# Optimization experiments

Measured on AMD Instinct MI355X. Metric: run time of the kernel, lower is better.

Reference implementation:

```python
import jax, jax.numpy as jnp
import numpy as np

SIGMA_AGG = 0.5
NUM_SEG = 33  # labels in [0, 32]; 0 = background


def setup_inputs() -> dict:
    key = jax.random.key(0)
    k1, k2, k3, k4, k5 = jax.random.split(key, 5)
    B, C, H, W = 16, 4, 736, 736
    return {
        "pred_similarities": jax.random.normal(k1, (B, C, H, W), dtype=jnp.float32),
        "regions_mask": jax.random.uniform(k2, (B, 1, H, W), dtype=jnp.float32),
        "kernels_mask": jax.random.uniform(k3, (B, 1, H, W), dtype=jnp.float32),
        "text_mask_ndi_labels": jax.random.randint(k4, (B, 1, H, W), 0, NUM_SEG, dtype=jnp.int32),
        "kernel_mask_ndi_labels": jax.random.randint(k5, (B, 1, H, W), 0, NUM_SEG, dtype=jnp.int32),
    }


def _per_batch(pred, rmask, kmask, rlab, klab):
    # pred: [C, N]; rmask/kmask: [N]; rlab/klab: [N] int
    # Per-kernel-label sum of kernels_mask, scattered back; 0 where label==0.
    ksum = jax.ops.segment_sum(kmask, klab, num_segments=NUM_SEG)            # [S]
    kcard = jnp.where(klab > 0, ksum[klab], 0.0)                              # [N]
    # Per-kernel-label sum of pred_similarities per channel.
    psum = jax.ops.segment_sum(pred.T, klab, num_segments=NUM_SEG)            # [S, C]
    Gk = jnp.where(klab[None, :] > 0, psum[klab].T, 0.0)                      # [C, N]
    # Region cardinality: faithful to source, it sums kernels_mask (not regions_mask)
    # over region labels.
    rsum = jax.ops.segment_sum(kmask, rlab, num_segments=NUM_SEG)             # [S]
    rcard = jnp.where(rlab > 0, rsum[rlab], 0.0)                              # [N]
    return kcard, Gk, rcard


def reference(pred_similarities, regions_mask, kernels_mask,
              text_mask_ndi_labels, kernel_mask_ndi_labels):
    B, C, H, W = pred_similarities.shape
    N = H * W
    pred = pred_similarities.reshape(B, C, N)
    rmask = regions_mask.reshape(B, N)
    kmask = kernels_mask.reshape(B, N)
    rlab = text_mask_ndi_labels.reshape(B, N)
    klab = kernel_mask_ndi_labels.reshape(B, N)

    kcard, Gk, rcard = jax.vmap(_per_batch)(pred, rmask, kmask, rlab, klab)
    # kcard/rcard: [B, N], Gk: [B, C, N]

    Gk = Gk / (kcard[:, None, :] + 1.0)
    Fp = pred * rmask[:, None, :]
    norm = jnp.sqrt(jnp.sum((Fp - Gk) ** 2, axis=1))                          # [B, N]
    d = jnp.maximum(norm - SIGMA_AGG, 0.0)
    D_p_K = jnp.log(d ** 2 + 1.0) / (rcard + 1.0)
    # Faithful to source bug: num_kernel is the LAST batch's max kernel label.
    num_kernel = klab[-1].max().astype(D_p_K.dtype)
    L_agg = (D_p_K / num_kernel).sum()
    return L_agg
```

## Files before the change

### kernel.cpp

```cpp
#include <hip/hip_runtime.h>
#include <hip/hip_cooperative_groups.h>

namespace cg = cooperative_groups;


constexpr int NSEG = 33;
constexpr int NCH  = 4;
constexpr int WS_PER_B = NSEG * (NCH + 2);
constexpr float SIGMA_AGG = 0.5f;
constexpr float QSCALE = 32768.0f;
constexpr float QINV   = 1.0f / 32768.0f;
constexpr float P8SCALE = 16.0f;
constexpr float P8INV   = 1.0f / 16.0f;

constexpr int NUMK_OFF = 16 * WS_PER_B;
constexpr int PART_OFF = 3200;

constexpr int BX    = 32;
constexpr int BTH   = 256;
constexpr int NITER = 17;

__device__ __forceinline__ int q8(float x) {
    int q = __float2int_rn(x * P8SCALE);
    return min(max(q, -127), 127) & 255;
}
__device__ __forceinline__ int pk8(float a, float b, float c, float d) {
    return q8(a) | (q8(b) << 8) | (q8(c) << 16) | (q8(d) << 24);
}
__device__ __forceinline__ float sx8(int w, int k) {
    return (float)((w << (24 - 8 * k)) >> 24);
}
__device__ __forceinline__ int pk16(int lo, int hi) {
    return (lo & 0xFFFF) | (hi << 16);
}

__global__ __launch_bounds__(BTH, 2) void fused_kernel(
    const float* __restrict__ pred, const float* __restrict__ rmask,
    const float* __restrict__ kmask, const int* __restrict__ rlab,
    const int* __restrict__ klab, int* __restrict__ ws,
    int* __restrict__ numk_out, float* __restrict__ partials,
    int N, int ncol, int lastB)
{
    const int b   = blockIdx.y;
    const int bx  = blockIdx.x;
    const int tid = threadIdx.x;

    __shared__ int   s_acc[WS_PER_B];
    __shared__ uint  s_lab[NITER][BTH][2];
    __shared__ float s_gk[NCH * NSEG];
    __shared__ float s_rinv[NSEG];
    __shared__ float s_part[4];
    for (int j = tid; j < WS_PER_B; j += BTH) s_acc[j] = 0;
    __syncthreads();

    const int Nv = N >> 2;
    const float4* __restrict__ predv = (const float4*)(pred + (size_t)b * NCH * N);
    const float4* __restrict__ kmv   = (const float4*)(kmask + (size_t)b * N);
    const int4*   __restrict__ rlv   = (const int4*)(rlab + (size_t)b * N);
    const int4*   __restrict__ klv   = (const int4*)(klab + (size_t)b * N);

    int rp8[NITER][4];

    int mk = 0;
    #pragma unroll
    for (int it = 0; it < NITER; ++it) {
        const int col = it * BX + bx;
        if (col < ncol) {
            const int i = col * BTH + tid;
            float4 km = kmv[i];
            int4   kl = klv[i];
            int4   rl = rlv[i];
            float4 p0 = predv[0 * Nv + i];
            float4 p1 = predv[1 * Nv + i];
            float4 p2 = predv[2 * Nv + i];
            float4 p3 = predv[3 * Nv + i];

            #define PIX(sfx) do {                                             \
                int kl_ = kl.sfx, rl_ = rl.sfx;                               \
                int kq = __float2int_rn(km.sfx * QSCALE);                     \
                atomicAdd(&s_acc[kl_], kq);                                   \
                atomicAdd(&s_acc[NSEG + rl_], kq);                            \
                atomicAdd(&s_acc[2 * NSEG + 0 * NSEG + kl_],                  \
                          __float2int_rn(p0.sfx * QSCALE));                   \
                atomicAdd(&s_acc[2 * NSEG + 1 * NSEG + kl_],                  \
                          __float2int_rn(p1.sfx * QSCALE));                   \
                atomicAdd(&s_acc[2 * NSEG + 2 * NSEG + kl_],                  \
                          __float2int_rn(p2.sfx * QSCALE));                   \
                atomicAdd(&s_acc[2 * NSEG + 3 * NSEG + kl_],                  \
                          __float2int_rn(p3.sfx * QSCALE));                   \
                mk = max(mk, kl_);                                            \
            } while (0)
            PIX(x); PIX(y); PIX(z); PIX(w);
            #undef PIX

            rp8[it][0] = pk8(p0.x, p1.x, p2.x, p3.x);
            rp8[it][1] = pk8(p0.y, p1.y, p2.y, p3.y);
            rp8[it][2] = pk8(p0.z, p1.z, p2.z, p3.z);
            rp8[it][3] = pk8(p0.w, p1.w, p2.w, p3.w);
            s_lab[it][tid][0] = (uint)pk16(kl.x | (rl.x << 6),
                                           kl.y | (rl.y << 6));
            s_lab[it][tid][1] = (uint)pk16(kl.z | (rl.z << 6),
                                           kl.w | (rl.w << 6));
        }
    }
    __syncthreads();

    int* wsb = ws + b * WS_PER_B;
    for (int j = tid; j < WS_PER_B; j += BTH)
        atomicAdd(&wsb[j], s_acc[j]);

    if (b == lastB) {
        for (int off = 32; off > 0; off >>= 1)
            mk = max(mk, __shfl_down(mk, off));
        if ((tid & 63) == 0) atomicMax(numk_out, mk);
    }

    cg::this_grid().sync();

    for (int j = tid; j < NSEG; j += BTH) {
        int rv = __hip_atomic_load(&wsb[NSEG + j], __ATOMIC_RELAXED,
                                   __HIP_MEMORY_SCOPE_AGENT);
        float rs = (float)rv * QINV;
        s_rinv[j] = (j > 0) ? 1.0f / (rs + 1.0f) : 1.0f;
    }
    for (int j = tid; j < NCH * NSEG; j += BTH) {
        int s  = j % NSEG;
        int kv = __hip_atomic_load(&wsb[s], __ATOMIC_RELAXED,
                                   __HIP_MEMORY_SCOPE_AGENT);
        int pv = __hip_atomic_load(&wsb[2 * NSEG + j], __ATOMIC_RELAXED,
                                   __HIP_MEMORY_SCOPE_AGENT);
        float ks = (float)kv * QINV;
        float ps = (float)pv * QINV;
        s_gk[j] = (s > 0) ? ps / (ks + 1.0f) : 0.0f;
    }
    __syncthreads();

    const float4* __restrict__ rmv = (const float4*)(rmask + (size_t)b * N);
    float acc = 0.0f;
    #pragma unroll
    for (int it = 0; it < NITER; ++it) {
        const int col = it * BX + bx;
        if (col < ncol) {
            const int i = col * BTH + tid;
            float4 rm = rmv[i];
            uint lw0 = s_lab[it][tid][0];
            uint lw1 = s_lab[it][tid][1];
            #define PIXR(w, lab16, rm_) do {                             \
                int kl_ = (lab16) & 63, rl_ = ((lab16) >> 6) & 63;       \
                float rmn = (rm_) * P8INV;                               \
                float d0 = fmaf(sx8(w, 0), rmn, -s_gk[0 * NSEG + kl_]);  \
                float d1 = fmaf(sx8(w, 1), rmn, -s_gk[1 * NSEG + kl_]);  \
                float d2 = fmaf(sx8(w, 2), rmn, -s_gk[2 * NSEG + kl_]);  \
                float d3 = fmaf(sx8(w, 3), rmn, -s_gk[3 * NSEG + kl_]);  \
                float ss = d0*d0 + d1*d1 + d2*d2 + d3*d3;                \
                float nrm = sqrtf(ss);                                   \
                float dd = fmaxf(nrm - SIGMA_AGG, 0.0f);                 \
                acc += __logf(fmaf(dd, dd, 1.0f)) * s_rinv[rl_];         \
            } while (0)
            PIXR(rp8[it][0], (int)(lw0 & 0xFFFF), rm.x);
            PIXR(rp8[it][1], (int)(lw0 >> 16),    rm.y);
            PIXR(rp8[it][2], (int)(lw1 & 0xFFFF), rm.z);
            PIXR(rp8[it][3], (int)(lw1 >> 16),    rm.w);
            #undef PIXR
        }
    }

    for (int off = 32; off > 0; off >>= 1)
        acc += __shfl_down(acc, off);
    if ((tid & 63) == 0) s_part[tid >> 6] = acc;
    __syncthreads();
    if (tid == 0)
        partials[b * BX + bx] = s_part[0] + s_part[1] + s_part[2] + s_part[3];
}

__global__ __launch_bounds__(256) void seg_sums_kernel(
    const float* __restrict__ pred, const float* __restrict__ kmask,
    const int* __restrict__ rlab, const int* __restrict__ klab,
    int* __restrict__ ws, int* __restrict__ numk_out, int N, int lastB)
{
    const int b = blockIdx.y;
    __shared__ int s_acc[WS_PER_B];
    __shared__ int s_maxk;
    for (int j = threadIdx.x; j < WS_PER_B; j += blockDim.x) s_acc[j] = 0;
    if (threadIdx.x == 0) s_maxk = 0;
    __syncthreads();

    const size_t bN = (size_t)b * N;
    const int Nv = N >> 2;
    const float4* __restrict__ predv = (const float4*)(pred + (size_t)b * NCH * N);
    const float4* __restrict__ kmv   = (const float4*)(kmask + bN);
    const int4*   __restrict__ rlv   = (const int4*)(rlab + bN);
    const int4*   __restrict__ klv   = (const int4*)(klab + bN);

    int mk = 0;
    for (int i = blockIdx.x * blockDim.x + threadIdx.x; i < Nv;
         i += gridDim.x * blockDim.x) {
        float4 km = kmv[i];
        int4   kl = klv[i];
        int4   rl = rlv[i];
        float4 p0 = predv[0 * Nv + i];
        float4 p1 = predv[1 * Nv + i];
        float4 p2 = predv[2 * Nv + i];
        float4 p3 = predv[3 * Nv + i];
        #define PIX(sfx) do {                                                 \
            int kl_ = kl.sfx, rl_ = rl.sfx;                                   \
            int kq = __float2int_rn(km.sfx * QSCALE);                         \
            atomicAdd(&s_acc[kl_], kq);                                       \
            atomicAdd(&s_acc[NSEG + rl_], kq);                                \
            atomicAdd(&s_acc[2 * NSEG + 0 * NSEG + kl_],                      \
                      __float2int_rn(p0.sfx * QSCALE));                       \
            atomicAdd(&s_acc[2 * NSEG + 1 * NSEG + kl_],                      \
                      __float2int_rn(p1.sfx * QSCALE));                       \
            atomicAdd(&s_acc[2 * NSEG + 2 * NSEG + kl_],                      \
                      __float2int_rn(p2.sfx * QSCALE));                       \
            atomicAdd(&s_acc[2 * NSEG + 3 * NSEG + kl_],                      \
                      __float2int_rn(p3.sfx * QSCALE));                       \
            mk = max(mk, kl_);                                                \
        } while (0)
        PIX(x); PIX(y); PIX(z); PIX(w);
        #undef PIX
    }
    __syncthreads();
    int* wsb = ws + b * WS_PER_B;
    for (int j = threadIdx.x; j < WS_PER_B; j += blockDim.x)
        atomicAdd(&wsb[j], s_acc[j]);
    if (b == lastB) {
        atomicMax(&s_maxk, mk);
        __syncthreads();
        if (threadIdx.x == 0) atomicMax(numk_out, s_maxk);
    }
}

__global__ __launch_bounds__(256) void loss_legacy_kernel(
    const float* __restrict__ pred, const float* __restrict__ rmask,
    const int* __restrict__ rlab, const int* __restrict__ klab,
    const int* __restrict__ ws, float* __restrict__ partials, int N)
{
    __shared__ float s_gk[NCH * NSEG];
    __shared__ float s_rinv[NSEG];
    __shared__ float s_part[4];
    const int* wsb = ws + blockIdx.y * WS_PER_B;
    for (int j = threadIdx.x; j < NSEG; j += blockDim.x) {
        float rs = (float)wsb[NSEG + j] * QINV;
        s_rinv[j] = (j > 0) ? 1.0f / (rs + 1.0f) : 1.0f;
    }
    for (int j = threadIdx.x; j < NCH * NSEG; j += blockDim.x) {
        int s = j % NSEG;
        float ks = (float)wsb[s] * QINV;
        float ps = (float)wsb[2 * NSEG + j] * QINV;
        s_gk[j] = (s > 0) ? ps / (ks + 1.0f) : 0.0f;
    }
    __syncthreads();

    const int b = blockIdx.y;
    const size_t bN = (size_t)b * N;
    const int Nv = N >> 2;
    const float4* __restrict__ predv = (const float4*)(pred + (size_t)b * NCH * N);
    const float4* __restrict__ rmv   = (const float4*)(rmask + bN);
    const int4*   __restrict__ rlv   = (const int4*)(rlab + bN);
    const int4*   __restrict__ klv   = (const int4*)(klab + bN);

    float acc = 0.0f;
    for (int i = blockIdx.x * blockDim.x + threadIdx.x; i < Nv;
         i += gridDim.x * blockDim.x) {
        float4 rm = rmv[i];
        int4   kl = klv[i];
        int4   rl = rlv[i];
        float4 p0 = predv[0 * Nv + i];
        float4 p1 = predv[1 * Nv + i];
        float4 p2 = predv[2 * Nv + i];
        float4 p3 = predv[3 * Nv + i];
        #define PIX(sfx) do {                                        \
            int kl_ = kl.sfx, rl_ = rl.sfx; float rm_ = rm.sfx;      \
            float d0 = fmaf(p0.sfx, rm_, -s_gk[0 * NSEG + kl_]);     \
            float d1 = fmaf(p1.sfx, rm_, -s_gk[1 * NSEG + kl_]);     \
            float d2 = fmaf(p2.sfx, rm_, -s_gk[2 * NSEG + kl_]);     \
            float d3 = fmaf(p3.sfx, rm_, -s_gk[3 * NSEG + kl_]);     \
            float ss = d0*d0 + d1*d1 + d2*d2 + d3*d3;                \
            float nrm = sqrtf(ss);                                   \
            float dd = fmaxf(nrm - SIGMA_AGG, 0.0f);                 \
            acc += __logf(fmaf(dd, dd, 1.0f)) * s_rinv[rl_];         \
        } while (0)
        PIX(x); PIX(y); PIX(z); PIX(w);
        #undef PIX
    }
    for (int off = 32; off > 0; off >>= 1) acc += __shfl_down(acc, off);
    if ((threadIdx.x & 63) == 0) s_part[threadIdx.x >> 6] = acc;
    __syncthreads();
    if (threadIdx.x == 0)
        partials[blockIdx.y * gridDim.x + blockIdx.x] =
            s_part[0] + s_part[1] + s_part[2] + s_part[3];
}

__global__ __launch_bounds__(256) void finalize_kernel(
    const float* __restrict__ partials, const int* __restrict__ numk,
    float* __restrict__ out, int nPart)
{
    __shared__ float s_part[4];
    float a = 0.0f;
    for (int i = threadIdx.x; i < nPart; i += blockDim.x) a += partials[i];
    for (int off = 32; off > 0; off >>= 1)
        a += __shfl_down(a, off);
    if ((threadIdx.x & 63) == 0) s_part[threadIdx.x >> 6] = a;
    __syncthreads();
    if (threadIdx.x == 0)
        out[0] = (s_part[0] + s_part[1] + s_part[2] + s_part[3]) / (float)(*numk);
}

extern "C" void kernel_launch(void* const* d_in, const int* in_sizes, int n_in,
                              void* d_out, int out_size, void* d_ws, size_t ws_size,
                              hipStream_t stream)
{
    const float* pred  = (const float*)d_in[0];
    const float* rmask = (const float*)d_in[1];
    const float* kmask = (const float*)d_in[2];
    const int*   rlab  = (const int*)d_in[3];
    const int*   klab  = (const int*)d_in[4];
    float* out = (float*)d_out;

    const int B = 16;
    int N = in_sizes[1] / B;

    int* wsi = (int*)d_ws;
    int* numk = wsi + NUMK_OFF;
    float* partials = (float*)(wsi + PART_OFF);

    hipMemsetAsync(d_ws, 0, (size_t)(NUMK_OFF + 1) * sizeof(int), stream);

    const int Nv = N >> 2;
    int ncol = (Nv > 0) ? Nv / BTH : 0;
    int lastB = B - 1;
    bool coop_ok = (N % 4 == 0) && (Nv % BTH == 0) && (ncol <= NITER * BX);

    if (coop_ok) {
        int dev = 0, maxBlk = 0, nCU = 0;
        if (hipGetDevice(&dev) != hipSuccess) coop_ok = false;
        if (coop_ok &&
            hipOccupancyMaxActiveBlocksPerMultiprocessor(
                &maxBlk, fused_kernel, BTH, 0) != hipSuccess) coop_ok = false;
        if (coop_ok &&
            hipDeviceGetAttribute(&nCU, hipDeviceAttributeMultiprocessorCount,
                                  dev) != hipSuccess) coop_ok = false;
        if (coop_ok && (long)maxBlk * nCU < (long)BX * B) coop_ok = false;
    }

    bool launched = false;
    if (coop_ok) {
        void* args[] = {
            (void*)&pred, (void*)&rmask, (void*)&kmask, (void*)&rlab,
            (void*)&klab, (void*)&wsi, (void*)&numk, (void*)&partials,
            (void*)&N, (void*)&ncol, (void*)&lastB,
        };
        if (hipLaunchCooperativeKernel((void*)fused_kernel, dim3(BX, B),
                                       dim3(BTH), args, 0, stream) == hipSuccess)
            launched = true;
    }

    if (launched) {
        finalize_kernel<<<dim3(1), dim3(256), 0, stream>>>(partials, numk, out,
                                                           BX * B);
    } else {
        dim3 block(256);
        dim3 grid(256, B);
        seg_sums_kernel<<<grid, block, 0, stream>>>(pred, kmask, rlab, klab,
                                                    wsi, numk, N, lastB);
        loss_legacy_kernel<<<grid, block, 0, stream>>>(pred, rmask, rlab, klab,
                                                       wsi, partials, N);
        finalize_kernel<<<dim3(1), block, 0, stream>>>(partials, numk, out,
                                                       256 * B);
    }
}
```

Measured before the change: 326.3 us.

## Replace cooperative grid sync with atomic spin barrier and double grid blocks

Drops the cooperative launch and cg grid sync in favour of a hand-rolled atomic counter barrier in workspace, launched with a normal kernel launch. It also doubles the blocks per batch (BX 32→64), halves the per-thread label cache (NITER 17→9) and raises the launch-bounds occupancy hint to 4 blocks per CU. The aim is lower launch and grid-sync overhead plus more parallelism and occupancy. The trade-off is that the occupancy check is gone, so the spin barrier can deadlock if all 1024 blocks cannot be resident at once, and the higher occupancy target may cause register pressure.

```diff
diff --git a/kernel.cpp b/kernel.cpp
--- a/kernel.cpp
+++ b/kernel.cpp
@@ -1,7 +1,4 @@
 #include <hip/hip_runtime.h>
-#include <hip/hip_cooperative_groups.h>
-
-namespace cg = cooperative_groups;
 
 
 constexpr int NSEG = 33;
@@ -14,11 +11,12 @@
 constexpr float P8INV   = 1.0f / 16.0f;
 
 constexpr int NUMK_OFF = 16 * WS_PER_B;
+constexpr int BAR_OFF  = NUMK_OFF + 1;
 constexpr int PART_OFF = 3200;
 
-constexpr int BX    = 32;
+constexpr int BX    = 64;
 constexpr int BTH   = 256;
-constexpr int NITER = 17;
+constexpr int NITER = 9;
 
 __device__ __forceinline__ int q8(float x) {
     int q = __float2int_rn(x * P8SCALE);
@@ -34,12 +32,12 @@
     return (lo & 0xFFFF) | (hi << 16);
 }
 
-__global__ __launch_bounds__(BTH, 2) void fused_kernel(
+__global__ __launch_bounds__(BTH, 4) void fused_kernel(
     const float* __restrict__ pred, const float* __restrict__ rmask,
     const float* __restrict__ kmask, const int* __restrict__ rlab,
     const int* __restrict__ klab, int* __restrict__ ws,
-    int* __restrict__ numk_out, float* __restrict__ partials,
-    int N, int ncol, int lastB)
+    int* __restrict__ numk_out, int* __restrict__ bar,
+    float* __restrict__ partials, int N, int ncol, int lastB, int nblk)
 {
     const int b   = blockIdx.y;
     const int bx  = blockIdx.x;
@@ -115,7 +113,15 @@
         if ((tid & 63) == 0) atomicMax(numk_out, mk);
     }
 
-    cg::this_grid().sync();
+    __syncthreads();
+    if (tid == 0) {
+        __hip_atomic_fetch_add(bar, 1, __ATOMIC_ACQ_REL,
+                               __HIP_MEMORY_SCOPE_AGENT);
+        while (__hip_atomic_load(bar, __ATOMIC_ACQUIRE,
+                                 __HIP_MEMORY_SCOPE_AGENT) < nblk)
+            __builtin_amdgcn_s_sleep(8);
+    }
+    __syncthreads();
 
     for (int j = tid; j < NSEG; j += BTH) {
         int rv = __hip_atomic_load(&wsb[NSEG + j], __ATOMIC_RELAXED,
@@ -323,40 +329,22 @@
 
     int* wsi = (int*)d_ws;
     int* numk = wsi + NUMK_OFF;
+    int* bar  = wsi + BAR_OFF;
     float* partials = (float*)(wsi + PART_OFF);
 
-    hipMemsetAsync(d_ws, 0, (size_t)(NUMK_OFF + 1) * sizeof(int), stream);
+    hipMemsetAsync(d_ws, 0, (size_t)(NUMK_OFF + 2) * sizeof(int), stream);
 
     const int Nv = N >> 2;
     int ncol = (Nv > 0) ? Nv / BTH : 0;
     int lastB = B - 1;
-    bool coop_ok = (N % 4 == 0) && (Nv % BTH == 0) && (ncol <= NITER * BX);
-
-    if (coop_ok) {
-        int dev = 0, maxBlk = 0, nCU = 0;
-        if (hipGetDevice(&dev) != hipSuccess) coop_ok = false;
-        if (coop_ok &&
-            hipOccupancyMaxActiveBlocksPerMultiprocessor(
-                &maxBlk, fused_kernel, BTH, 0) != hipSuccess) coop_ok = false;
-        if (coop_ok &&
-            hipDeviceGetAttribute(&nCU, hipDeviceAttributeMultiprocessorCount,
-                                  dev) != hipSuccess) coop_ok = false;
-        if (coop_ok && (long)maxBlk * nCU < (long)BX * B) coop_ok = false;
-    }
-
-    bool launched = false;
-    if (coop_ok) {
-        void* args[] = {
-            (void*)&pred, (void*)&rmask, (void*)&kmask, (void*)&rlab,
-            (void*)&klab, (void*)&wsi, (void*)&numk, (void*)&partials,
-            (void*)&N, (void*)&ncol, (void*)&lastB,
-        };
-        if (hipLaunchCooperativeKernel((void*)fused_kernel, dim3(BX, B),
-                                       dim3(BTH), args, 0, stream) == hipSuccess)
-            launched = true;
-    }
-
-    if (launched) {
+    int nblk = BX * B;
+    const bool fused_ok = (N % 4 == 0) && (Nv % BTH == 0) &&
+                          (ncol <= NITER * BX);
+
+    if (fused_ok) {
+        fused_kernel<<<dim3(BX, B), dim3(BTH), 0, stream>>>(
+            pred, rmask, kmask, rlab, klab, wsi, numk, bar, partials,
+            N, ncol, lastB, nblk);
         finalize_kernel<<<dim3(1), dim3(256), 0, stream>>>(partials, numk, out,
                                                            BX * B);
     } else {
```

Result: slower. 430.3 us (+31.9%).
